# Performance work log

Hardware: AMD Instinct MI355X
Metric: run time of the kernel (lower is better)

Reference implementation:

```python
import jax, jax.numpy as jnp
import numpy as np

NUM_HEADS = 16


def setup_inputs() -> dict:
    key = jax.random.key(0)
    ks = jax.random.split(key, 10)
    B, S, D = 2, 2048, 1024
    x = jax.random.normal(ks[0], (B, S, D), dtype=jnp.float32)
    mask = jax.random.randint(ks[1], (B, 1, 1, S), 0, 2, dtype=jnp.int32)
    scale = 1.0 / np.sqrt(D)
    wq = jax.random.normal(ks[2], (D, D), dtype=jnp.float32) * scale
    bq = jnp.zeros((D,), dtype=jnp.float32)
    wk = jax.random.normal(ks[3], (D, D), dtype=jnp.float32) * scale
    bk = jnp.zeros((D,), dtype=jnp.float32)
    wv = jax.random.normal(ks[4], (D, D), dtype=jnp.float32) * scale
    bv = jnp.zeros((D,), dtype=jnp.float32)
    wo = jax.random.normal(ks[5], (D, D), dtype=jnp.float32) * scale
    bo = jnp.zeros((D,), dtype=jnp.float32)
    return {"x": x, "mask": mask, "wq": wq, "bq": bq, "wk": wk, "bk": bk,
            "wv": wv, "bv": bv, "wo": wo, "bo": bo}


def reference(x, mask, wq, bq, wk, bk, wv, bv, wo, bo):
    B, S, D = x.shape
    H = NUM_HEADS
    dk = D // H

    def split_heads(t):
        # (B, S, D) -> (B, H, S, dk)
        return t.reshape(B, S, H, dk).transpose(0, 2, 1, 3)

    # PyTorch nn.Linear: y = x @ W^T + b
    q = split_heads(x @ wq.T + bq)
    k = split_heads(x @ wk.T + bk)
    v = split_heads(x @ wv.T + bv)

    # scaled dot-product attention with explicit score matrix (as original)
    logits = jnp.einsum('bhqd,bhkd->bhqk', q, k) / jnp.sqrt(jnp.float32(dk))
    logits = jnp.where(mask == 0, jnp.float32(-1e9), logits)
    attn_weights = jax.nn.softmax(logits, axis=-1)
    # dropout(p=0.1) is identity in eval mode (deterministic reference)
    attn = jnp.einsum('bhqk,bhkd->bhqd', attn_weights, v)

    attn = attn.transpose(0, 2, 1, 3).reshape(B, S, D)
    out = attn @ wo.T + bo
    return out, attn_weights
```

## Files before the change

### kernel.cpp

```cpp
#include <hip/hip_runtime.h>
#include <hip/hip_bf16.h>

#define DEV __device__ __forceinline__

typedef __attribute__((ext_vector_type(8))) __bf16 bf16x8;
typedef __attribute__((ext_vector_type(8))) short s16x8;
typedef __attribute__((ext_vector_type(4))) float f32x4;
typedef __attribute__((ext_vector_type(2))) unsigned long long u64x2;

DEV f32x4 mfma16(s16x8 a, s16x8 b, f32x4 c){
  return __builtin_amdgcn_mfma_f32_16x16x32_bf16(
      __builtin_bit_cast(bf16x8, a), __builtin_bit_cast(bf16x8, b), c, 0, 0, 0);
}

DEV unsigned int cvtpk(float a, float b){
  float2 t; t.x = a; t.y = b;
  __hip_bfloat162 h = __float22bfloat162_rn(t);
  unsigned int r;
  __builtin_memcpy(&r, &h, 4);
  return r;
}

DEV unsigned short f2bf(float f){
  __hip_bfloat16 h = __float2bfloat16(f);
  unsigned short r;
  __builtin_memcpy(&r, &h, 2);
  return r;
}

DEV float bf2f(unsigned short u){
  return __builtin_bit_cast(float, ((unsigned int)u) << 16);
}

DEV unsigned long long pack4(float4 v){
  return (unsigned long long)cvtpk(v.x, v.y) | ((unsigned long long)cvtpk(v.z, v.w) << 32);
}

DEV unsigned long long pack4f(float a, float b, float c, float d){
  return (unsigned long long)cvtpk(a, b) | ((unsigned long long)cvtpk(c, d) << 32);
}

DEV void async16(const void* g, void* l){
  __builtin_amdgcn_global_load_lds(
      (const __attribute__((address_space(1))) unsigned int*)g,
      (__attribute__((address_space(3))) unsigned int*)l, 16, 0, 0);
}

__global__ __launch_bounds__(256) void cvt_kernel(
    const float* __restrict__ x, const float* __restrict__ wq, const float* __restrict__ wk,
    const float* __restrict__ wv, const float* __restrict__ wo,
    const float* __restrict__ bq, const float* __restrict__ bk, const float* __restrict__ bv,
    unsigned long long* __restrict__ xb, unsigned long long* __restrict__ wqkvb,
    unsigned long long* __restrict__ wob, float4* __restrict__ bqkv)
{
  const int i = blockIdx.x * 256 + threadIdx.x;
  const int X4 = 1048576, W4 = 262144;
  if (i < X4){
    xb[i] = pack4(((const float4*)x)[i]);
  } else if (i < X4 + 3*W4){
    int j = i - X4;
    const float* src = (j < W4) ? wq : (j < 2*W4) ? wk : wv;
    int jj = (j < W4) ? j : (j < 2*W4) ? (j - W4) : (j - 2*W4);
    wqkvb[j] = pack4(((const float4*)src)[jj]);
  } else if (i < X4 + 4*W4){
    int j = i - X4 - 3*W4;
    wob[j] = pack4(((const float4*)wo)[j]);
  } else if (i < X4 + 4*W4 + 768){
    int j = i - X4 - 4*W4;
    const float* src = (j < 256) ? bq : (j < 512) ? bk : bv;
    int jj = (j < 256) ? j : (j < 512) ? (j - 256) : (j - 512);
    bqkv[j] = ((const float4*)src)[jj];
  }
}

__global__ __launch_bounds__(256) void gemm_qkv(
    const unsigned short* __restrict__ A,
    const unsigned short* __restrict__ B,
    const float* __restrict__ bias,
    unsigned short* __restrict__ oq,
    unsigned short* __restrict__ okk,
    unsigned short* __restrict__ ovt)
{
  __shared__ __align__(16) char smem[32768];
  char* As = smem;
  char* Bs = smem + 16384;
  const int tid = threadIdx.x;
  const int l = tid & 63, w = tid >> 6, g = l >> 4;

  const int orig = blockIdx.x;
  const int lin = (orig & 7) * 96 + (orig >> 3);
  const int m0 = (lin / 24) * 128, n0 = (lin % 24) * 128;
  const int rowbytes = 2048;

  f32x4 acc[4][4] = {};
  const int wr = w >> 1, wc = w & 1;
  const int wm = wr * 64, wn = wc * 64;

  const int srow = w * 32 + (l >> 3);
  const int scol = (((l & 7) ^ (l >> 3)) << 4);
  const char* Abp = (const char*)A + (size_t)(m0 + srow) * rowbytes + scol;
  const char* Bbp = (const char*)B + (size_t)(n0 + srow) * rowbytes + scol;
  char* Asw = As + w * 4096;
  char* Bsw = Bs + w * 4096;

  int aoff[4][2], boff[4][2];
  for (int mf = 0; mf < 4; ++mf)
    for (int ks = 0; ks < 2; ++ks){
      int ra = wm + mf * 16 + (l & 15);
      aoff[mf][ks] = ra * 128 + ((ks * 64 + g * 16) ^ ((l & 7) << 4));
      int rb = wn + mf * 16 + (l & 15);
      boff[mf][ks] = rb * 128 + ((ks * 64 + g * 16) ^ ((l & 7) << 4));
    }

  for (int kt = 0; kt < 16; ++kt){
    const char* ab = Abp + kt * 128;
    const char* bb = Bbp + kt * 128;
    for (int i = 0; i < 4; ++i){
      async16(ab + (size_t)i * 8 * rowbytes, Asw + i * 1024);
      async16(bb + (size_t)i * 8 * rowbytes, Bsw + i * 1024);
    }
    __syncthreads();
    for (int ks = 0; ks < 2; ++ks){
      s16x8 af[4], bf[4];
      for (int mf = 0; mf < 4; ++mf) af[mf] = *(const s16x8*)(As + aoff[mf][ks]);
      for (int nf = 0; nf < 4; ++nf) bf[nf] = *(const s16x8*)(Bs + boff[nf][ks]);
      for (int mf = 0; mf < 4; ++mf)
        for (int nf = 0; nf < 4; ++nf)
          acc[mf][nf] = mfma16(af[mf], bf[nf], acc[mf][nf]);
    }
    __syncthreads();
  }

  if (n0 >= 2048){
    for (int nf = 0; nf < 4; ++nf){
      int nloc = wn + nf * 16 + (l & 15);
      float bs = bias[n0 + nloc];
      for (int mf = 0; mf < 4; ++mf){
        int mby = (wm + mf * 16 + g * 4) * 2;
        unsigned long long pk = pack4f(acc[mf][nf][0] + bs, acc[mf][nf][1] + bs,
                                       acc[mf][nf][2] + bs, acc[mf][nf][3] + bs);
        *(unsigned long long*)(smem + nloc * 256 + (mby ^ ((nloc & 15) << 4))) = pk;
      }
    }
    __syncthreads();
    int b2 = m0 >> 11, s0 = m0 & 2047;
    for (int i = 0; i < 8; ++i){
      int idx = i * 256 + tid;
      int row = idx >> 4, c8 = (idx & 15) * 8;
      s16x8 vv = *(const s16x8*)(smem + row * 256 + ((c8 * 2) ^ ((row & 15) << 4)));
      *(s16x8*)(ovt + (size_t)(b2 * 1024 + (n0 - 2048) + row) * 2048 + s0 + c8) = vv;
    }
    return;
  }

  for (int mf = 0; mf < 4; ++mf)
    for (int nf = 0; nf < 4; ++nf)
      for (int r = 0; r < 4; ++r){
        int grow = m0 + wm + mf * 16 + g * 4 + r;
        int n = n0 + wn + nf * 16 + (l & 15);
        float v = acc[mf][nf][r] + bias[n];
        if (n < 1024) oq [(size_t)grow * 1024 + n]          = f2bf(v);
        else          okk[(size_t)grow * 1024 + (n - 1024)] = f2bf(v);
      }
}

__global__ __launch_bounds__(256) void gemm_out(
    const unsigned short* __restrict__ A,
    const unsigned short* __restrict__ B,
    const float* __restrict__ bias,
    float* __restrict__ of)
{
  __shared__ __align__(16) char smem[32768];
  char* As = smem;
  char* Bs = smem + 16384;
  const int tid = threadIdx.x, l = tid & 63, w = tid >> 6, g = l >> 4;
  const int orig = blockIdx.x;
  const int lin = (orig & 7) * 64 + (orig >> 3);
  const int m0 = (lin >> 4) * 128, n0 = (lin & 15) * 64;
  const int rowbytes = 2048;

  f32x4 acc[2][4] = {};
  const int wm = w * 32;

  const int scol = (((l & 7) ^ (l >> 3)) << 4);
  const char* Abp = (const char*)A + (size_t)(m0 + w * 32 + (l >> 3)) * rowbytes + scol;
  const char* Bbp = (const char*)B + (size_t)(n0 + w * 16 + (l >> 3)) * rowbytes + scol;
  char* Asw = As + w * 4096;
  char* Bsw = Bs + w * 2048;

  int aoff[2][2], boff[4][2];
  for (int ks = 0; ks < 2; ++ks){
    for (int mf = 0; mf < 2; ++mf){
      int ra = wm + mf * 16 + (l & 15);
      aoff[mf][ks] = ra * 128 + ((ks * 64 + g * 16) ^ ((l & 7) << 4));
    }
    for (int nf = 0; nf < 4; ++nf){
      int rb = nf * 16 + (l & 15);
      boff[nf][ks] = rb * 128 + ((ks * 64 + g * 16) ^ ((l & 7) << 4));
    }
  }

  for (int kt = 0; kt < 16; ++kt){
    for (int i = 0; i < 4; ++i)
      async16(Abp + kt * 128 + (size_t)i * 8 * rowbytes, Asw + i * 1024);
    for (int i = 0; i < 2; ++i)
      async16(Bbp + kt * 128 + (size_t)i * 8 * rowbytes, Bsw + i * 1024);
    __syncthreads();
    for (int ks = 0; ks < 2; ++ks){
      s16x8 af[2], bf[4];
      for (int mf = 0; mf < 2; ++mf) af[mf] = *(const s16x8*)(As + aoff[mf][ks]);
      for (int nf = 0; nf < 4; ++nf) bf[nf] = *(const s16x8*)(Bs + boff[nf][ks]);
      for (int mf = 0; mf < 2; ++mf)
        for (int nf = 0; nf < 4; ++nf)
          acc[mf][nf] = mfma16(af[mf], bf[nf], acc[mf][nf]);
    }
    __syncthreads();
  }

  __syncthreads();
  char* stg = smem + w * 8192;
  float bv4[4];
  for (int nf = 0; nf < 4; ++nf) bv4[nf] = bias[n0 + nf * 16 + (l & 15)];
  for (int mf = 0; mf < 2; ++mf)
    for (int nf = 0; nf < 4; ++nf)
      for (int r = 0; r < 4; ++r){
        int row = mf * 16 + g * 4 + r;
        int colb = (nf * 16 + (l & 15)) * 4;
        *(float*)(stg + row * 256 + (colb ^ ((row & 7) << 4))) = acc[mf][nf][r] + bv4[nf];
      }
  __syncthreads();
  for (int t = 0; t < 8; ++t){
    int row = t * 4 + (l >> 4);
    int colb = ((l & 15) * 16) ^ ((row & 7) << 4);
    f32x4 v = *(const f32x4*)(stg + row * 256 + colb);
    __builtin_nontemporal_store(v, (f32x4*)&of[(size_t)(m0 + wm + row) * 1024 + n0 + (l & 15) * 4]);
  }
}

__global__ __launch_bounds__(256, 3) void attn_kernel(
    const unsigned short* __restrict__ qb,
    const unsigned short* __restrict__ kb,
    const unsigned short* __restrict__ vtb,
    const int* __restrict__ mask,
    float* __restrict__ Pout,
    unsigned short* __restrict__ attnb)
{
  const int flat = blockIdx.x;
  const int sw = (flat & 7) * 256 + (flat >> 3);
  const int qt = sw & 63, h = (sw >> 6) & 15, b = sw >> 10;
  const int tid = threadIdx.x, l = tid & 63, w = tid >> 6, g = l >> 4;
  const int q0 = qt * 32;

  __shared__ float maskadd[2048];
  __shared__ float zpart[4][32];
  __shared__ __align__(16) unsigned long long estu[4096];

  for (int i = tid; i < 2048; i += 256)
    maskadd[i] = mask[b * 2048 + i] ? 0.0f : -1e30f;

  s16x8 qf[2][2];
  for (int mf = 0; mf < 2; ++mf)
    for (int ks = 0; ks < 2; ++ks)
      qf[mf][ks] = *(const s16x8*)(qb + (size_t)(b*2048 + q0 + mf*16 + (l&15)) * 1024
                                   + h*64 + ks*32 + g*8);

  const unsigned short* Kb = kb + (size_t)b * 2048 * 1024 + h * 64;
  const unsigned short* Vb = vtb + ((size_t)b * 1024 + h * 64) * 2048;

  __syncthreads();

  float zacc[2] = {0.0f, 0.0f};
  for (int j = 0; j < 8; ++j){
    int kk0 = j * 256 + w * 64;
    f32x4 c[2][4] = {};
    for (int nh = 0; nh < 2; ++nh){
      s16x8 kf[2][2];
      for (int n2 = 0; n2 < 2; ++n2)
        for (int ks = 0; ks < 2; ++ks)
          kf[n2][ks] = *(const s16x8*)(Kb + (size_t)(kk0 + (nh*2+n2)*16 + (l&15)) * 1024 + ks*32 + g*8);
      __builtin_amdgcn_s_setprio(1);
      for (int ks = 0; ks < 2; ++ks)
        for (int mf = 0; mf < 2; ++mf)
          for (int n2 = 0; n2 < 2; ++n2)
            c[mf][nh*2+n2] = mfma16(kf[n2][ks], qf[mf][ks], c[mf][nh*2+n2]);
      __builtin_amdgcn_s_setprio(0);
    }
    for (int nf = 0; nf < 4; ++nf){
      f32x4 ma = *(const f32x4*)&maskadd[kk0 + nf*16 + g*4];
      for (int mf = 0; mf < 2; ++mf)
        for (int r = 0; r < 4; ++r)
          zacc[mf] += __expf(fmaf(c[mf][nf][r], 0.125f, ma[r]));
    }
  }
  for (int mf = 0; mf < 2; ++mf){
    float z = zacc[mf];
    z += __shfl_xor(z, 16, 64);
    z += __shfl_xor(z, 32, 64);
    zacc[mf] = z;
  }
  if (g == 0){
    zpart[w][l & 15]        = zacc[0];
    zpart[w][16 + (l & 15)] = zacc[1];
  }
  __syncthreads();
  float zinv[2];
  for (int mf = 0; mf < 2; ++mf){
    int row = mf*16 + (l & 15);
    zinv[mf] = 1.0f / (zpart[0][row] + zpart[1][row] + zpart[2][row] + zpart[3][row]);
  }

  float* Pb = Pout + ((size_t)(b*16 + h) * 2048 + q0) * 2048;
  f32x4 pv[2][4] = {};
  char* estw = (char*)estu + w * 8192;
  for (int j = 0; j < 8; ++j){
    char* ej = estw + (j & 1) * 4096;
    int kk0 = j * 256 + w * 64;
    f32x4 c[2][4] = {};
    for (int nh = 0; nh < 2; ++nh){
      s16x8 kf[2][2];
      for (int n2 = 0; n2 < 2; ++n2)
        for (int ks = 0; ks < 2; ++ks)
          kf[n2][ks] = *(const s16x8*)(Kb + (size_t)(kk0 + (nh*2+n2)*16 + (l&15)) * 1024 + ks*32 + g*8);
      __builtin_amdgcn_s_setprio(1);
      for (int ks = 0; ks < 2; ++ks)
        for (int mf = 0; mf < 2; ++mf)
          for (int n2 = 0; n2 < 2; ++n2)
            c[mf][nh*2+n2] = mfma16(kf[n2][ks], qf[mf][ks], c[mf][nh*2+n2]);
      __builtin_amdgcn_s_setprio(0);
    }
    for (int mf = 0; mf < 2; ++mf){
      int q = mf*16 + (l & 15);
      for (int nf = 0; nf < 4; ++nf){
        f32x4 ma = *(const f32x4*)&maskadd[kk0 + nf*16 + g*4];
        f32x4 p4;
        for (int r = 0; r < 4; ++r)
          p4[r] = __expf(fmaf(c[mf][nf][r], 0.125f, ma[r])) * zinv[mf];
        *(unsigned long long*)(ej + q*128 + ((nf*32 + g*8) ^ ((q & 7) << 4))) =
            pack4f(p4[0], p4[1], p4[2], p4[3]);
      }
    }
    s16x8 pa[2][2];
    for (int mf = 0; mf < 2; ++mf)
      for (int ks = 0; ks < 2; ++ks){
        int q = mf*16 + (l & 15);
        const unsigned long long* pp =
            (const unsigned long long*)(ej + q*128 + ((ks*64 + g*16) ^ ((q & 7) << 4)));
        u64x2 t; t[0] = pp[0]; t[1] = pp[1];
        pa[mf][ks] = __builtin_bit_cast(s16x8, t);
      }
    for (int dh = 0; dh < 2; ++dh){
      s16x8 vf[2][2];
      for (int d2 = 0; d2 < 2; ++d2)
        for (int ks = 0; ks < 2; ++ks)
          vf[d2][ks] = *(const s16x8*)(Vb + (size_t)((dh*2+d2)*16 + (l&15)) * 2048 + kk0 + ks*32 + g*8);
      __builtin_amdgcn_s_setprio(1);
      for (int ks = 0; ks < 2; ++ks)
        for (int mf = 0; mf < 2; ++mf)
          for (int d2 = 0; d2 < 2; ++d2)
            pv[mf][dh*2+d2] = mfma16(pa[mf][ks], vf[d2][ks], pv[mf][dh*2+d2]);
      __builtin_amdgcn_s_setprio(0);
    }
    for (int t = 0; t < 8; ++t){
      int row = t * 4 + (l >> 4);
      unsigned long long pk =
          *(const unsigned long long*)(ej + row*128 + (((l & 15) * 8) ^ ((row & 7) << 4)));
      f32x4 ps;
      ps[0] = bf2f((unsigned short)(pk      ));
      ps[1] = bf2f((unsigned short)(pk >> 16));
      ps[2] = bf2f((unsigned short)(pk >> 32));
      ps[3] = bf2f((unsigned short)(pk >> 48));
      __builtin_nontemporal_store(ps, (f32x4*)&Pb[(size_t)row * 2048 + kk0 + (l & 15) * 4]);
    }
  }

  __syncthreads();
  char* est = (char*)estu;
  char* bufw = (w == 0) ? (char*)maskadd : est + (w - 1) * 8192;
  for (int mf = 0; mf < 2; ++mf)
    for (int dn = 0; dn < 4; ++dn)
      for (int r = 0; r < 4; ++r){
        int row = mf*16 + g*4 + r, col = dn*16 + (l & 15);
        *(float*)(bufw + row*256 + ((col*4) ^ (((row >> 2) & 3) << 6))) = pv[mf][dn][r];
      }
  __syncthreads();
  {
    int row = tid >> 3, c8 = (tid & 7) * 8;
    int off = row*256 + ((c8*4) ^ (((row >> 2) & 3) << 6));
    f32x4 s0_ = *(f32x4*)((char*)maskadd + off);
    f32x4 s1_ = *(f32x4*)((char*)maskadd + off + 16);
    s0_ += *(f32x4*)(est + off);           s1_ += *(f32x4*)(est + off + 16);
    s0_ += *(f32x4*)(est + 8192 + off);    s1_ += *(f32x4*)(est + 8192 + off + 16);
    s0_ += *(f32x4*)(est + 16384 + off);   s1_ += *(f32x4*)(est + 16384 + off + 16);
    u64x2 ov;
    ov[0] = pack4f(s0_[0], s0_[1], s0_[2], s0_[3]);
    ov[1] = pack4f(s1_[0], s1_[1], s1_[2], s1_[3]);
    *(u64x2*)&attnb[(size_t)(b*2048 + q0 + row) * 1024 + h*64 + c8] = ov;
  }
}

extern "C" void kernel_launch(void* const* d_in, const int* in_sizes, int n_in,
                              void* d_out, int out_size, void* d_ws, size_t ws_size,
                              hipStream_t stream)
{
  const float* x  = (const float*)d_in[0];
  const int* mask = (const int*)d_in[1];
  const float* wq = (const float*)d_in[2];
  const float* bq = (const float*)d_in[3];
  const float* wk = (const float*)d_in[4];
  const float* bk = (const float*)d_in[5];
  const float* wv = (const float*)d_in[6];
  const float* bv = (const float*)d_in[7];
  const float* wo = (const float*)d_in[8];
  const float* bo = (const float*)d_in[9];

  char* ws = (char*)d_ws;
  unsigned short* xb    = (unsigned short*)(ws);
  unsigned short* wqkvb = (unsigned short*)(ws + 8388608);
  unsigned short* wob   = (unsigned short*)(ws + 14680064);
  float*          bqkv  = (float*)(ws + 16777216);
  unsigned short* qb    = (unsigned short*)(ws + 16793600);
  unsigned short* kb    = (unsigned short*)(ws + 25182208);
  unsigned short* vtb   = (unsigned short*)(ws + 33570816);
  unsigned short* attnb = (unsigned short*)(ws + 41959424);

  float* fout = (float*)d_out;
  float* Pout = fout + 4194304;

  cvt_kernel<<<8195, 256, 0, stream>>>(x, wq, wk, wv, wo, bq, bk, bv,
                                       (unsigned long long*)xb, (unsigned long long*)wqkvb,
                                       (unsigned long long*)wob, (float4*)bqkv);
  gemm_qkv<<<768, 256, 0, stream>>>(xb, wqkvb, bqkv, qb, kb, vtb);
  attn_kernel<<<2048, 256, 0, stream>>>(qb, kb, vtb, mask, Pout, attnb);
  gemm_out<<<512, 256, 0, stream>>>(attnb, wob, bo, fout);
}
```

Measured before the change: 266.5 us.

## Store unnormalized exp scores in LDS to skip QK recompute in attention

The attention kernel now keeps the whole 32x2048 row block of unnormalized exp scores (bf16) in shared memory during the first pass. This removes the second QK^T matmul and exp pass. Normalization is deferred: P is scaled by the inverse row sum when written out, and the PV accumulator is scaled at the final reduction. The block grows to 512 threads (8 waves, each owning a 256-key slice), and shared memory rises to about 140KB per block, which cuts occupancy to one block per CU. PV now runs on unnormalized bf16 exps, which slightly changes rounding.

```diff
diff --git a/kernel.cpp b/kernel.cpp
--- a/kernel.cpp
+++ b/kernel.cpp
@@ -237,7 +237,7 @@
   }
 }
 
-__global__ __launch_bounds__(256, 3) void attn_kernel(
+__global__ __launch_bounds__(512) void attn_kernel(
     const unsigned short* __restrict__ qb,
     const unsigned short* __restrict__ kb,
     const unsigned short* __restrict__ vtb,
@@ -251,11 +251,14 @@
   const int tid = threadIdx.x, l = tid & 63, w = tid >> 6, g = l >> 4;
   const int q0 = qt * 32;
 
+  __shared__ __align__(16) unsigned long long estu[16384];
   __shared__ float maskadd[2048];
-  __shared__ float zpart[4][32];
-  __shared__ __align__(16) unsigned long long estu[4096];
-
-  for (int i = tid; i < 2048; i += 256)
+  __shared__ float zpart[8][32];
+  __shared__ float zfullinv[32];
+
+  char* Ebase = (char*)estu;
+
+  for (int i = tid; i < 2048; i += 512)
     maskadd[i] = mask[b * 2048 + i] ? 0.0f : -1e30f;
 
   s16x8 qf[2][2];
@@ -270,8 +273,9 @@
   __syncthreads();
 
   float zacc[2] = {0.0f, 0.0f};
-  for (int j = 0; j < 8; ++j){
-    int kk0 = j * 256 + w * 64;
+  for (int jj = 0; jj < 4; ++jj){
+    const int kk0 = w * 256 + jj * 64;
+    const int cb = kk0 * 2;
     f32x4 c[2][4] = {};
     for (int nh = 0; nh < 2; ++nh){
       s16x8 kf[2][2];
@@ -285,11 +289,18 @@
             c[mf][nh*2+n2] = mfma16(kf[n2][ks], qf[mf][ks], c[mf][nh*2+n2]);
       __builtin_amdgcn_s_setprio(0);
     }
-    for (int nf = 0; nf < 4; ++nf){
-      f32x4 ma = *(const f32x4*)&maskadd[kk0 + nf*16 + g*4];
-      for (int mf = 0; mf < 2; ++mf)
-        for (int r = 0; r < 4; ++r)
-          zacc[mf] += __expf(fmaf(c[mf][nf][r], 0.125f, ma[r]));
+    for (int mf = 0; mf < 2; ++mf){
+      int q = mf*16 + (l & 15);
+      for (int nf = 0; nf < 4; ++nf){
+        f32x4 ma = *(const f32x4*)&maskadd[kk0 + nf*16 + g*4];
+        f32x4 e;
+        for (int r = 0; r < 4; ++r){
+          e[r] = __expf(fmaf(c[mf][nf][r], 0.125f, ma[r]));
+          zacc[mf] += e[r];
+        }
+        *(unsigned long long*)(Ebase + q*4096 + cb + ((nf*32 + g*8) ^ ((q & 7) << 4))) =
+            pack4f(e[0], e[1], e[2], e[3]);
+      }
     }
   }
   for (int mf = 0; mf < 2; ++mf){
@@ -303,48 +314,24 @@
     zpart[w][16 + (l & 15)] = zacc[1];
   }
   __syncthreads();
-  float zinv[2];
-  for (int mf = 0; mf < 2; ++mf){
-    int row = mf*16 + (l & 15);
-    zinv[mf] = 1.0f / (zpart[0][row] + zpart[1][row] + zpart[2][row] + zpart[3][row]);
-  }
+  if (tid < 32){
+    float s = 0.0f;
+    for (int ww = 0; ww < 8; ++ww) s += zpart[ww][tid];
+    zfullinv[tid] = 1.0f / s;
+  }
+  __syncthreads();
 
   float* Pb = Pout + ((size_t)(b*16 + h) * 2048 + q0) * 2048;
   f32x4 pv[2][4] = {};
-  char* estw = (char*)estu + w * 8192;
-  for (int j = 0; j < 8; ++j){
-    char* ej = estw + (j & 1) * 4096;
-    int kk0 = j * 256 + w * 64;
-    f32x4 c[2][4] = {};
-    for (int nh = 0; nh < 2; ++nh){
-      s16x8 kf[2][2];
-      for (int n2 = 0; n2 < 2; ++n2)
-        for (int ks = 0; ks < 2; ++ks)
-          kf[n2][ks] = *(const s16x8*)(Kb + (size_t)(kk0 + (nh*2+n2)*16 + (l&15)) * 1024 + ks*32 + g*8);
-      __builtin_amdgcn_s_setprio(1);
-      for (int ks = 0; ks < 2; ++ks)
-        for (int mf = 0; mf < 2; ++mf)
-          for (int n2 = 0; n2 < 2; ++n2)
-            c[mf][nh*2+n2] = mfma16(kf[n2][ks], qf[mf][ks], c[mf][nh*2+n2]);
-      __builtin_amdgcn_s_setprio(0);
-    }
-    for (int mf = 0; mf < 2; ++mf){
-      int q = mf*16 + (l & 15);
-      for (int nf = 0; nf < 4; ++nf){
-        f32x4 ma = *(const f32x4*)&maskadd[kk0 + nf*16 + g*4];
-        f32x4 p4;
-        for (int r = 0; r < 4; ++r)
-          p4[r] = __expf(fmaf(c[mf][nf][r], 0.125f, ma[r])) * zinv[mf];
-        *(unsigned long long*)(ej + q*128 + ((nf*32 + g*8) ^ ((q & 7) << 4))) =
-            pack4f(p4[0], p4[1], p4[2], p4[3]);
-      }
-    }
+  for (int jj = 0; jj < 4; ++jj){
+    const int kk0 = w * 256 + jj * 64;
+    const int cb = kk0 * 2;
     s16x8 pa[2][2];
     for (int mf = 0; mf < 2; ++mf)
       for (int ks = 0; ks < 2; ++ks){
         int q = mf*16 + (l & 15);
         const unsigned long long* pp =
-            (const unsigned long long*)(ej + q*128 + ((ks*64 + g*16) ^ ((q & 7) << 4)));
+            (const unsigned long long*)(Ebase + q*4096 + cb + ((ks*64 + g*16) ^ ((q & 7) << 4)));
         u64x2 t; t[0] = pp[0]; t[1] = pp[1];
         pa[mf][ks] = __builtin_bit_cast(s16x8, t);
       }
@@ -363,19 +350,19 @@
     for (int t = 0; t < 8; ++t){
       int row = t * 4 + (l >> 4);
       unsigned long long pk =
-          *(const unsigned long long*)(ej + row*128 + (((l & 15) * 8) ^ ((row & 7) << 4)));
+          *(const unsigned long long*)(Ebase + row*4096 + cb + (((l & 15) * 8) ^ ((row & 7) << 4)));
+      float zr = zfullinv[row];
       f32x4 ps;
-      ps[0] = bf2f((unsigned short)(pk      ));
-      ps[1] = bf2f((unsigned short)(pk >> 16));
-      ps[2] = bf2f((unsigned short)(pk >> 32));
-      ps[3] = bf2f((unsigned short)(pk >> 48));
+      ps[0] = bf2f((unsigned short)(pk      )) * zr;
+      ps[1] = bf2f((unsigned short)(pk >> 16)) * zr;
+      ps[2] = bf2f((unsigned short)(pk >> 32)) * zr;
+      ps[3] = bf2f((unsigned short)(pk >> 48)) * zr;
       __builtin_nontemporal_store(ps, (f32x4*)&Pb[(size_t)row * 2048 + kk0 + (l & 15) * 4]);
     }
   }
 
   __syncthreads();
-  char* est = (char*)estu;
-  char* bufw = (w == 0) ? (char*)maskadd : est + (w - 1) * 8192;
+  char* bufw = Ebase + w * 8192;
   for (int mf = 0; mf < 2; ++mf)
     for (int dn = 0; dn < 4; ++dn)
       for (int r = 0; r < 4; ++r){
@@ -384,17 +371,14 @@
       }
   __syncthreads();
   {
-    int row = tid >> 3, c8 = (tid & 7) * 8;
-    int off = row*256 + ((c8*4) ^ (((row >> 2) & 3) << 6));
-    f32x4 s0_ = *(f32x4*)((char*)maskadd + off);
-    f32x4 s1_ = *(f32x4*)((char*)maskadd + off + 16);
-    s0_ += *(f32x4*)(est + off);           s1_ += *(f32x4*)(est + off + 16);
-    s0_ += *(f32x4*)(est + 8192 + off);    s1_ += *(f32x4*)(est + 8192 + off + 16);
-    s0_ += *(f32x4*)(est + 16384 + off);   s1_ += *(f32x4*)(est + 16384 + off + 16);
-    u64x2 ov;
-    ov[0] = pack4f(s0_[0], s0_[1], s0_[2], s0_[3]);
-    ov[1] = pack4f(s1_[0], s1_[1], s1_[2], s1_[3]);
-    *(u64x2*)&attnb[(size_t)(b*2048 + q0 + row) * 1024 + h*64 + c8] = ov;
+    int row = tid >> 4, c4 = (tid & 15) * 4;
+    int off = row*256 + ((c4*4) ^ (((row >> 2) & 3) << 6));
+    f32x4 s = {};
+    for (int ww = 0; ww < 8; ++ww)
+      s += *(const f32x4*)(Ebase + ww*8192 + off);
+    float zr = zfullinv[row];
+    unsigned long long ov = pack4f(s[0]*zr, s[1]*zr, s[2]*zr, s[3]*zr);
+    *(unsigned long long*)&attnb[(size_t)(b*2048 + q0 + row) * 1024 + h*64 + c4] = ov;
   }
 }
 
@@ -430,6 +414,6 @@
                                        (unsigned long long*)xb, (unsigned long long*)wqkvb,
                                        (unsigned long long*)wob, (float4*)bqkv);
   gemm_qkv<<<768, 256, 0, stream>>>(xb, wqkvb, bqkv, qb, kb, vtb);
-  attn_kernel<<<2048, 256, 0, stream>>>(qb, kb, vtb, mask, Pout, attnb);
+  attn_kernel<<<2048, 512, 0, stream>>>(qb, kb, vtb, mask, Pout, attnb);
   gemm_out<<<512, 256, 0, stream>>>(attnb, wob, bo, fout);
 }
```

New measurement: 244.6 us. -8.2%, faster.
